# Kernel tuning notes

Hardware: AMD Instinct MI355X
Metric: run time of the kernel (lower is better)

The kernel has to match this reference:

```python
import jax, jax.numpy as jnp
import numpy as np

N, E = 100000, 600000
IN, H = 164, 128
NH = 4  # attention heads over embed_dim H//4 = 32


def layer_norm(x, g, b, eps=1e-5):
    m = x.mean(-1, keepdims=True)
    v = x.var(-1, keepdims=True)
    return (x - m) * jax.lax.rsqrt(v + eps) * g + b


def gcn_conv(x, W, b, src, dst, n):
    # PyG GCNConv: add self-loops, symmetric D^{-1/2}(A+I)D^{-1/2} normalization.
    deg = jnp.ones((n,), x.dtype).at[dst].add(1.0)  # degree of A+I on target nodes
    dinv = jax.lax.rsqrt(deg)
    xw = x @ W  # [n, out]
    msg = xw[src] * (dinv[src] * dinv[dst])[:, None]  # gather + edge-norm
    agg = jax.ops.segment_sum(msg, dst, num_segments=n)  # scatter-add
    agg = agg + xw * (dinv * dinv)[:, None]  # self-loop term
    return agg + b


def mha_seq1(x, Wq, bq, Wk, bk, Wv, bv, Wo, bo):
    # nn.MultiheadAttention with seq_len==1: softmax over a single key -> weights==1.
    dh = x.shape[-1] // NH
    q = (x @ Wq + bq).reshape(-1, NH, dh)
    k = (x @ Wk + bk).reshape(-1, NH, dh)
    v = (x @ Wv + bv).reshape(-1, NH, dh)
    scores = jnp.sum(q * k, -1, keepdims=True) / jnp.sqrt(jnp.float32(dh))  # [n,NH,1]
    attn = jax.nn.softmax(scores[..., None], axis=-1)[..., 0]  # all ones, kept for fidelity
    out = (attn * v).reshape(-1, NH * dh)
    return out @ Wo + bo


def setup_inputs() -> dict:
    key = jax.random.key(0)
    ks = jax.random.split(key, 16)

    def kaiming(k, i, o):
        return jax.random.normal(k, (i, o), jnp.float32) * (2.0 / i) ** 0.5

    Ha, Hb, Hc = H, H // 2, H // 4  # 128, 64, 32
    return {
        "x": jax.random.normal(ks[0], (N, IN), jnp.float32),
        "edge_index": jax.random.randint(ks[1], (2, E), 0, N),
        "Wi": kaiming(ks[2], IN, Ha), "bi": jnp.zeros((Ha,), jnp.float32),
        "g1": jnp.ones((Ha,), jnp.float32), "b1": jnp.zeros((Ha,), jnp.float32),
        "Wg1": kaiming(ks[3], Ha, Ha), "bg1": jnp.zeros((Ha,), jnp.float32),
        "Wg2": kaiming(ks[4], Ha, Hb), "bg2": jnp.zeros((Hb,), jnp.float32),
        "g2": jnp.ones((Hb,), jnp.float32), "b2": jnp.zeros((Hb,), jnp.float32),
        "Wg3": kaiming(ks[5], Hb, Hc), "bg3": jnp.zeros((Hc,), jnp.float32),
        "Wq": kaiming(ks[6], Hc, Hc), "bq": jnp.zeros((Hc,), jnp.float32),
        "Wk": kaiming(ks[7], Hc, Hc), "bk": jnp.zeros((Hc,), jnp.float32),
        "Wv": kaiming(ks[8], Hc, Hc), "bv": jnp.zeros((Hc,), jnp.float32),
        "Wo": kaiming(ks[9], Hc, Hc), "bo": jnp.zeros((Hc,), jnp.float32),
        "Wc1": kaiming(ks[10], Hc, H // 8), "bc1": jnp.zeros((H // 8,), jnp.float32),
        "Wc2": kaiming(ks[11], H // 8, 32), "bc2": jnp.zeros((32,), jnp.float32),
        "Wc3": kaiming(ks[12], 32, 1), "bc3": jnp.zeros((1,), jnp.float32),
    }


def reference(x, edge_index, Wi, bi, g1, b1, Wg1, bg1, Wg2, bg2, g2, b2,
              Wg3, bg3, Wq, bq, Wk, bk, Wv, bv, Wo, bo,
              Wc1, bc1, Wc2, bc2, Wc3, bc3):
    src, dst = edge_index[0], edge_index[1]
    n = x.shape[0]
    # dropout layers are identity in eval mode
    h = layer_norm(jax.nn.relu(x @ Wi + bi), g1, b1)
    h1 = jax.nn.relu(gcn_conv(h, Wg1, bg1, src, dst, n)) + h
    h2 = layer_norm(jax.nn.relu(gcn_conv(h1, Wg2, bg2, src, dst, n)), g2, b2)
    h3 = jax.nn.relu(gcn_conv(h2, Wg3, bg3, src, dst, n))
    h3 = mha_seq1(h3, Wq, bq, Wk, bk, Wv, bv, Wo, bo)
    h3 = jax.nn.relu(h3 @ Wc1 + bc1)
    h3 = jax.nn.relu(h3 @ Wc2 + bc2)
    return (h3 @ Wc3 + bc3)[:, 0]
```

## Files before the change

kernel.cpp:

```cpp
#include <hip/hip_runtime.h>


typedef __attribute__((ext_vector_type(8))) _Float16 f16x8;
typedef __attribute__((ext_vector_type(4))) _Float16 f16x4;
typedef __attribute__((ext_vector_type(4))) float f32x4;

#define GLOAD_LDS16(gp, lp)                                        \
  __builtin_amdgcn_global_load_lds(                                \
      (const __attribute__((address_space(1))) void*)(gp),         \
      (__attribute__((address_space(3))) void*)(lp), 16, 0, 0)

static __device__ __forceinline__ void wait_vm0() {
  asm volatile("s_waitcnt vmcnt(0)" ::: "memory");
}
static __device__ __forceinline__ void wait_vm10() {
  asm volatile("s_waitcnt vmcnt(10)" ::: "memory");
}
static __device__ __forceinline__ void wait_vm5() {
  asm volatile("s_waitcnt vmcnt(5)" ::: "memory");
}
static __device__ __forceinline__ void wait_vm3() {
  asm volatile("s_waitcnt vmcnt(3)" ::: "memory");
}
static __device__ __forceinline__ void wait_lgkm0() {
  asm volatile("s_waitcnt lgkmcnt(0)" ::: "memory");
  __builtin_amdgcn_sched_barrier(0);
}

__global__ void k_count(const int* __restrict__ dst, int* __restrict__ counts, int e) {
  int i = blockIdx.x * blockDim.x + threadIdx.x;
  if (i < e) atomicAdd(&counts[dst[i]], 1);
}

__global__ __launch_bounds__(256) void k_scan_part(
    const int* __restrict__ counts, int* __restrict__ bsums, int n) {
  int tid = threadIdx.x;
  int i0 = blockIdx.x * 1024 + tid * 4;
  int s = 0;
#pragma unroll
  for (int k = 0; k < 4; k++) { int i = i0 + k; if (i < n) s += counts[i]; }
#pragma unroll
  for (int d = 1; d < 64; d <<= 1) s += __shfl_xor(s, d);
  __shared__ int wsum[4];
  int lane = tid & 63, w = tid >> 6;
  if (lane == 0) wsum[w] = s;
  __syncthreads();
  if (tid == 0) bsums[blockIdx.x] = wsum[0] + wsum[1] + wsum[2] + wsum[3];
}

__global__ __launch_bounds__(256) void k_scan_down(
    int* __restrict__ counts, const int* __restrict__ bsums,
    int* __restrict__ offsets, float* __restrict__ dinv, int n, int e, int nb) {
  int tid = threadIdx.x;
  int lane = tid & 63, w = tid >> 6;
  __shared__ int wsum[4], psum[4];
  int pv = (tid < nb && tid < blockIdx.x) ? bsums[tid] : 0;
#pragma unroll
  for (int d = 1; d < 64; d <<= 1) pv += __shfl_xor(pv, d);
  if (lane == 0) psum[w] = pv;
  __syncthreads();
  int blockpref = psum[0] + psum[1] + psum[2] + psum[3];

  int i0 = blockIdx.x * 1024 + tid * 4;
  int c[4]; int tsum = 0;
#pragma unroll
  for (int k = 0; k < 4; k++) { int i = i0 + k; c[k] = (i < n) ? counts[i] : 0; tsum += c[k]; }
  int v = tsum;
#pragma unroll
  for (int d = 1; d < 64; d <<= 1) { int t = __shfl_up(v, d); if (lane >= d) v += t; }
  if (lane == 63) wsum[w] = v;
  __syncthreads();
  int wadd = 0;
#pragma unroll
  for (int q = 0; q < 4; q++) if (q < w) wadd += wsum[q];
  int run = (v - tsum) + wadd + blockpref;
#pragma unroll
  for (int k = 0; k < 4; k++) {
    int i = i0 + k;
    if (i < n) {
      offsets[i] = run;
      dinv[i] = rsqrtf((float)(c[k] + 1));
      counts[i] = 0;
    }
    run += c[k];
  }
  if (blockIdx.x == 0 && tid == 0) offsets[n] = e;
}

__global__ void k_fill(const int* __restrict__ src, const int* __restrict__ dst,
                       const int* __restrict__ offsets, int* __restrict__ cursor,
                       const float* __restrict__ dinv, int2* __restrict__ csr, int e) {
  int i = blockIdx.x * blockDim.x + threadIdx.x;
  if (i >= e) return;
  int s = src[i], d = dst[i];
  int pos = atomicAdd(&cursor[d], 1);
  csr[offsets[d] + pos] = make_int2(s, __float_as_int(dinv[s] * dinv[d]));
}

__device__ __forceinline__ void pack_hi(const float* __restrict__ W,
                                        _Float16* __restrict__ dst,
                                        int K, int N, int u) {
  int lane = u & 63; int rest = u >> 6; int CT = N >> 4;
  int ct = rest % CT, ks = rest / CT;
  int gcol = ct * 16 + (lane & 15);
  int gk0 = ks * 32 + (lane >> 4) * 8;
  size_t o = (size_t)(ks * CT + ct) * 512 + lane * 8;
#pragma unroll
  for (int i = 0; i < 8; i++) {
    float v = (gk0 + i < K) ? W[(size_t)(gk0 + i) * N + gcol] : 0.0f;
    dst[o + i] = (_Float16)v;
  }
}

__global__ void k_setup(const float* __restrict__ Wi, const float* __restrict__ Wg1,
                        const float* __restrict__ Wg2, const float* __restrict__ Wg3,
                        _Float16* __restrict__ pWi, _Float16* __restrict__ pWg1,
                        _Float16* __restrict__ pWg2, _Float16* __restrict__ pWg3,
                        int* __restrict__ counts, float* __restrict__ zp, int n) {
  int b = blockIdx.x;
  if (b < 25) {
    int t = b * 256 + threadIdx.x;
    if (t < 3072) pack_hi(Wi, pWi, 164, 128, t);
    else if (t < 5120) pack_hi(Wg1, pWg1, 128, 128, t - 3072);
    else if (t < 6144) pack_hi(Wg2, pWg2, 128, 64, t - 5120);
    else if (t < 6400) pack_hi(Wg3, pWg3, 64, 32, t - 6144);
  } else {
    if (b == 25 && threadIdx.x < 64) zp[threadIdx.x] = 0.0f;
    int i = (b - 25) * 256 + threadIdx.x;
    if (i < n) counts[i] = 0;
  }
}

__global__ __launch_bounds__(512, 4) void k_gemm_in(
    const float* __restrict__ x, const _Float16* __restrict__ pB,
    const float* __restrict__ bias, const float* __restrict__ gamma,
    const float* __restrict__ beta, const float* __restrict__ zp,
    _Float16* __restrict__ out, int n) {
  constexpr int N = 128, CT = 8, KS = 6;
  __shared__ __align__(16) float sAi[8][2][512];
  int tid = threadIdx.x;
  int lane = tid & 63, w = tid >> 6;
  int rowbase = blockIdx.x * 128 + w * 16;
  const f16x8* Bf = (const f16x8*)pB;

  auto stage = [&](int ks, int buf) {
#pragma unroll
    for (int j = 0; j < 2; j++) {
      int r_ = j * 8 + (lane >> 3);
      int c_ = (lane & 7) ^ (lane >> 3);
      int rg = rowbase + r_;
      bool ok = (rg < n) && (ks < 5 || c_ == 0);
      const void* s = ok ? (const void*)(x + (size_t)rg * 164 + ks * 32 + c_ * 4)
                         : (const void*)zp;
      GLOAD_LDS16(s, &sAi[w][buf][j * 256]);
    }
  };

  f32x4 acc[CT];
#pragma unroll
  for (int c = 0; c < CT; c++) acc[c] = (f32x4)0.0f;

  int rr = lane & 15;
  int c0 = (lane >> 4) * 2;
  int s0 = c0 ^ (rr & 7);
  int s1 = (c0 + 1) ^ (rr & 7);

  f16x8 bfr[2][CT];
#pragma unroll
  for (int c = 0; c < CT; c++) bfr[0][c] = Bf[c * 64 + lane];
  stage(0, 0);

#pragma unroll
  for (int ks = 0; ks < KS; ks++) {
    if (ks + 1 < KS) {
#pragma unroll
      for (int c = 0; c < CT; c++)
        bfr[(ks + 1) & 1][c] = Bf[((ks + 1) * CT + c) * 64 + lane];
      stage(ks + 1, (ks + 1) & 1);
      wait_vm10();
    } else {
      wait_vm0();
    }
    const float* bp = &sAi[w][ks & 1][0];
    float4 u0 = *(const float4*)&bp[rr * 32 + s0 * 4];
    float4 u1 = *(const float4*)&bp[rr * 32 + s1 * 4];
    float v[8] = {u0.x, u0.y, u0.z, u0.w, u1.x, u1.y, u1.z, u1.w};
    f16x8 ah;
#pragma unroll
    for (int i = 0; i < 8; i++) ah[i] = (_Float16)v[i];
#pragma unroll
    for (int c = 0; c < CT; c++)
      acc[c] = __builtin_amdgcn_mfma_f32_16x16x32_f16(ah, bfr[ks & 1][c], acc[c], 0, 0, 0);
  }

  int r0 = (lane >> 4) * 4;
  int li = lane & 15;
  float s1v[4] = {0, 0, 0, 0}, s2v[4] = {0, 0, 0, 0};
#pragma unroll
  for (int c = 0; c < CT; c++) {
    float bb = bias[c * 16 + li];
#pragma unroll
    for (int r = 0; r < 4; r++) {
      float t = acc[c][r] + bb;
      t = t > 0.0f ? t : 0.0f;
      acc[c][r] = t;
      s1v[r] += t;
      s2v[r] += t * t;
    }
  }
#pragma unroll
  for (int m = 1; m < 16; m <<= 1) {
#pragma unroll
    for (int r = 0; r < 4; r++) {
      s1v[r] += __shfl_xor(s1v[r], m);
      s2v[r] += __shfl_xor(s2v[r], m);
    }
  }
  wait_lgkm0();
  _Float16* lr = (_Float16*)&sAi[w][0][0];
#pragma unroll
  for (int c = 0; c < CT; c++) {
    float gv = gamma[c * 16 + li], bv = beta[c * 16 + li];
#pragma unroll
    for (int r = 0; r < 4; r++) {
      float mean = s1v[r] * (1.0f / N);
      float var = s2v[r] * (1.0f / N) - mean * mean;
      float rs = rsqrtf(var + 1e-5f);
      lr[(r0 + r) * 128 + c * 16 + li] =
          (_Float16)((acc[c][r] - mean) * rs * gv + bv);
    }
  }
  wait_lgkm0();
#pragma unroll
  for (int i = 0; i < 4; i++) {
    int chunk = i * 64 + lane;
    int rloc = chunk >> 4;
    int cc = chunk & 15;
    if (rowbase + rloc < n)
      *(f16x8*)&out[(size_t)(rowbase + rloc) * 128 + cc * 8] =
          *(const f16x8*)&lr[chunk * 8];
  }
}

template <int K, int N>
__global__ __launch_bounds__(512, 4) void k_gemm_f16(
    const _Float16* __restrict__ A, const _Float16* __restrict__ pB,
    const float* __restrict__ zp, _Float16* __restrict__ out, int n) {
  constexpr int KS = K / 32, CT = N / 16;
  __shared__ __align__(16) _Float16 sA[8][2][512];
  __shared__ __align__(16) _Float16 sR[8][16 * N];
  int tid = threadIdx.x;
  int lane = tid & 63, w = tid >> 6;
  int rowbase = blockIdx.x * 128 + w * 16;
  const f16x8* Bf = (const f16x8*)pB;

  int r_ = lane >> 2;
  int c_ = (lane & 3) ^ (r_ & 3);
  int rg = rowbase + r_;
  const _Float16* asrc = A + (size_t)rg * K + c_ * 8;
  bool rok = rg < n;

  auto stage = [&](int ks, int buf) {
    const void* s = rok ? (const void*)(asrc + ks * 32) : (const void*)zp;
    GLOAD_LDS16(s, &sA[w][buf][0]);
  };

  f32x4 acc[CT];
#pragma unroll
  for (int c = 0; c < CT; c++) acc[c] = (f32x4)0.0f;

  int rr = lane & 15;
  int slot = (lane >> 4) ^ (rr & 3);

  f16x8 bfr[2][CT];
#pragma unroll
  for (int c = 0; c < CT; c++) bfr[0][c] = Bf[c * 64 + lane];
  stage(0, 0);

#pragma unroll
  for (int ks = 0; ks < KS; ks++) {
    if (ks + 1 < KS) {
#pragma unroll
      for (int c = 0; c < CT; c++)
        bfr[(ks + 1) & 1][c] = Bf[((ks + 1) * CT + c) * 64 + lane];
      stage(ks + 1, (ks + 1) & 1);
      if (CT == 8) wait_vm10(); else if (CT == 4) wait_vm5(); else wait_vm3();
    } else {
      wait_vm0();
    }
    f16x8 av = *(const f16x8*)&sA[w][ks & 1][rr * 32 + slot * 8];
#pragma unroll
    for (int c = 0; c < CT; c++)
      acc[c] = __builtin_amdgcn_mfma_f32_16x16x32_f16(av, bfr[ks & 1][c], acc[c], 0, 0, 0);
  }

  int r0 = (lane >> 4) * 4;
  int li = lane & 15;
  wait_lgkm0();
  _Float16* lr = &sR[w][0];
#pragma unroll
  for (int c = 0; c < CT; c++) {
#pragma unroll
    for (int r = 0; r < 4; r++)
      lr[(r0 + r) * N + c * 16 + li] = (_Float16)acc[c][r];
  }
  wait_lgkm0();
#pragma unroll
  for (int i = 0; i < N / 32; i++) {
    int chunk = i * 64 + lane;
    int rloc = chunk / (N / 8);
    int cc = chunk % (N / 8);
    if (rowbase + rloc < n)
      *(f16x8*)&out[(size_t)(rowbase + rloc) * N + cc * 8] =
          *(const f16x8*)&lr[chunk * 8];
  }
}

template <int OUT_D, int MODE>
__global__ __launch_bounds__(256, 2) void k_gather(
    const int* __restrict__ off, const int2* __restrict__ csr,
    const _Float16* __restrict__ xw, const float* __restrict__ dinv,
    const float* __restrict__ bias, const _Float16* __restrict__ auxh,
    const float* __restrict__ gamma, const float* __restrict__ beta,
    _Float16* __restrict__ out, int n) {
  constexpr int TPN = OUT_D / 4;
  constexpr int NPB = 256 / TPN;
  int tid = threadIdx.x;
  int node = blockIdx.x * NPB + tid / TPN;
  int li = tid % TPN;
  if (node >= n) return;
  int start = off[node], end = off[node + 1];
  float di = dinv[node];
  float d2 = di * di;
  const _Float16* xp = xw + 4 * li;
  f16x4 self = *(const f16x4*)(xp + (size_t)node * OUT_D);
  f16x4 hres;
  if constexpr (MODE == 0)
    hres = *(const f16x4*)(auxh + (size_t)node * OUT_D + 4 * li);
  float a0 = (float)self[0] * d2 + bias[4 * li + 0];
  float a1 = (float)self[1] * d2 + bias[4 * li + 1];
  float a2 = (float)self[2] * d2 + bias[4 * li + 2];
  float a3 = (float)self[3] * d2 + bias[4 * li + 3];
  for (int cb = start; cb < end; cb += TPN) {
    int m = end - cb; if (m > TPN) m = TPN;
    int sv = node; float nv = 0.0f;
    if (li < m) { int2 me = csr[cb + li]; sv = me.x; nv = __int_as_float(me.y); }
    for (int j0 = 0; j0 < m; j0 += 8) {
      int s0 = __shfl(sv, j0 + 0, TPN), s1 = __shfl(sv, j0 + 1, TPN);
      int s2 = __shfl(sv, j0 + 2, TPN), s3 = __shfl(sv, j0 + 3, TPN);
      int s4 = __shfl(sv, j0 + 4, TPN), s5 = __shfl(sv, j0 + 5, TPN);
      int s6 = __shfl(sv, j0 + 6, TPN), s7 = __shfl(sv, j0 + 7, TPN);
      float w0 = __shfl(nv, j0 + 0, TPN), w1 = __shfl(nv, j0 + 1, TPN);
      float w2 = __shfl(nv, j0 + 2, TPN), w3 = __shfl(nv, j0 + 3, TPN);
      float w4 = __shfl(nv, j0 + 4, TPN), w5 = __shfl(nv, j0 + 5, TPN);
      float w6 = __shfl(nv, j0 + 6, TPN), w7 = __shfl(nv, j0 + 7, TPN);
      f16x4 v0 = *(const f16x4*)(xp + (size_t)s0 * OUT_D);
      f16x4 v1 = *(const f16x4*)(xp + (size_t)s1 * OUT_D);
      f16x4 v2 = *(const f16x4*)(xp + (size_t)s2 * OUT_D);
      f16x4 v3 = *(const f16x4*)(xp + (size_t)s3 * OUT_D);
      f16x4 v4 = *(const f16x4*)(xp + (size_t)s4 * OUT_D);
      f16x4 v5 = *(const f16x4*)(xp + (size_t)s5 * OUT_D);
      f16x4 v6 = *(const f16x4*)(xp + (size_t)s6 * OUT_D);
      f16x4 v7 = *(const f16x4*)(xp + (size_t)s7 * OUT_D);
      a0 += (float)v0[0] * w0 + (float)v1[0] * w1 + (float)v2[0] * w2 + (float)v3[0] * w3
          + (float)v4[0] * w4 + (float)v5[0] * w5 + (float)v6[0] * w6 + (float)v7[0] * w7;
      a1 += (float)v0[1] * w0 + (float)v1[1] * w1 + (float)v2[1] * w2 + (float)v3[1] * w3
          + (float)v4[1] * w4 + (float)v5[1] * w5 + (float)v6[1] * w6 + (float)v7[1] * w7;
      a2 += (float)v0[2] * w0 + (float)v1[2] * w1 + (float)v2[2] * w2 + (float)v3[2] * w3
          + (float)v4[2] * w4 + (float)v5[2] * w5 + (float)v6[2] * w6 + (float)v7[2] * w7;
      a3 += (float)v0[3] * w0 + (float)v1[3] * w1 + (float)v2[3] * w2 + (float)v3[3] * w3
          + (float)v4[3] * w4 + (float)v5[3] * w5 + (float)v6[3] * w6 + (float)v7[3] * w7;
    }
  }
  _Float16* po = out + (size_t)node * OUT_D + 4 * li;
  if constexpr (MODE == 0) {
    f16x4 o;
    o[0] = (_Float16)((a0 > 0.0f ? a0 : 0.0f) + (float)hres[0]);
    o[1] = (_Float16)((a1 > 0.0f ? a1 : 0.0f) + (float)hres[1]);
    o[2] = (_Float16)((a2 > 0.0f ? a2 : 0.0f) + (float)hres[2]);
    o[3] = (_Float16)((a3 > 0.0f ? a3 : 0.0f) + (float)hres[3]);
    *(f16x4*)po = o;
  } else if constexpr (MODE == 1) {
    float v0 = a0 > 0.0f ? a0 : 0.0f, v1 = a1 > 0.0f ? a1 : 0.0f;
    float v2 = a2 > 0.0f ? a2 : 0.0f, v3 = a3 > 0.0f ? a3 : 0.0f;
    float s1 = v0 + v1 + v2 + v3;
    float s2 = v0 * v0 + v1 * v1 + v2 * v2 + v3 * v3;
#pragma unroll
    for (int d = 1; d < TPN; d <<= 1) {
      s1 += __shfl_xor(s1, d, TPN);
      s2 += __shfl_xor(s2, d, TPN);
    }
    float m_ = s1 * (1.0f / OUT_D);
    float var = s2 * (1.0f / OUT_D) - m_ * m_;
    float rs = rsqrtf(var + 1e-5f);
    f16x4 o;
    o[0] = (_Float16)((v0 - m_) * rs * gamma[4 * li + 0] + beta[4 * li + 0]);
    o[1] = (_Float16)((v1 - m_) * rs * gamma[4 * li + 1] + beta[4 * li + 1]);
    o[2] = (_Float16)((v2 - m_) * rs * gamma[4 * li + 2] + beta[4 * li + 2]);
    o[3] = (_Float16)((v3 - m_) * rs * gamma[4 * li + 3] + beta[4 * li + 3]);
    *(f16x4*)po = o;
  } else {
    f16x4 o;
    o[0] = (_Float16)a0; o[1] = (_Float16)a1;
    o[2] = (_Float16)a2; o[3] = (_Float16)a3;
    *(f16x4*)po = o;
  }
}

__global__ __launch_bounds__(256) void k_tail(
    const _Float16* __restrict__ agg3, const float* __restrict__ Wv,
    const float* __restrict__ bv, const float* __restrict__ Wo,
    const float* __restrict__ bo, const float* __restrict__ Wc1,
    const float* __restrict__ bc1, const float* __restrict__ Wc2,
    const float* __restrict__ bc2, const float* __restrict__ Wc3,
    const float* __restrict__ bc3, float* __restrict__ out, int n) {
  __shared__ float sWv[1024], sWo[1024], sWc1[512], sWc2[512];
  __shared__ float sbv[32], sbo[32], sbc2[32], sWc3[32], sbc1[16], sbc3[1];
  int tid = threadIdx.x;
  for (int i = tid; i < 1024; i += 256) { sWv[i] = Wv[i]; sWo[i] = Wo[i]; }
  for (int i = tid; i < 512; i += 256) { sWc1[i] = Wc1[i]; sWc2[i] = Wc2[i]; }
  if (tid < 32) { sbv[tid] = bv[tid]; sbo[tid] = bo[tid];
                  sbc2[tid] = bc2[tid]; sWc3[tid] = Wc3[tid]; }
  if (tid < 16) sbc1[tid] = bc1[tid];
  if (tid == 0) sbc3[0] = bc3[0];
  __syncthreads();
  int node = blockIdx.x * blockDim.x + tid;
  if (node >= n) return;
  float a[32];
  const f16x8* row8 = (const f16x8*)(agg3 + (size_t)node * 32);
#pragma unroll
  for (int q = 0; q < 4; q++) {
    f16x8 t = row8[q];
#pragma unroll
    for (int i = 0; i < 8; i++) {
      float f = (float)t[i];
      a[8 * q + i] = f > 0.0f ? f : 0.0f;
    }
  }
  float v[32];
#pragma unroll
  for (int j = 0; j < 32; j++) v[j] = sbv[j];
  for (int k = 0; k < 32; k++) {
#pragma unroll
    for (int j = 0; j < 32; j++) v[j] += a[k] * sWv[k * 32 + j];
  }
  float o[32];
#pragma unroll
  for (int j = 0; j < 32; j++) o[j] = sbo[j];
  for (int k = 0; k < 32; k++) {
#pragma unroll
    for (int j = 0; j < 32; j++) o[j] += v[k] * sWo[k * 32 + j];
  }
  float c1[16];
#pragma unroll
  for (int j = 0; j < 16; j++) c1[j] = sbc1[j];
  for (int k = 0; k < 32; k++) {
#pragma unroll
    for (int j = 0; j < 16; j++) c1[j] += o[k] * sWc1[k * 16 + j];
  }
#pragma unroll
  for (int j = 0; j < 16; j++) c1[j] = c1[j] > 0.0f ? c1[j] : 0.0f;
  float c2[32];
#pragma unroll
  for (int j = 0; j < 32; j++) c2[j] = sbc2[j];
  for (int k = 0; k < 16; k++) {
#pragma unroll
    for (int j = 0; j < 32; j++) c2[j] += c1[k] * sWc2[k * 32 + j];
  }
  float r = sbc3[0];
#pragma unroll
  for (int k = 0; k < 32; k++) {
    float c = c2[k] > 0.0f ? c2[k] : 0.0f;
    r += c * sWc3[k];
  }
  out[node] = r;
}

extern "C" void kernel_launch(void* const* d_in, const int* in_sizes, int n_in,
                              void* d_out, int out_size, void* d_ws, size_t ws_size,
                              hipStream_t stream) {
  const float* x   = (const float*)d_in[0];
  const int* ei    = (const int*)d_in[1];
  const float* Wi  = (const float*)d_in[2];
  const float* bi  = (const float*)d_in[3];
  const float* g1  = (const float*)d_in[4];
  const float* b1  = (const float*)d_in[5];
  const float* Wg1 = (const float*)d_in[6];
  const float* bg1 = (const float*)d_in[7];
  const float* Wg2 = (const float*)d_in[8];
  const float* bg2 = (const float*)d_in[9];
  const float* g2  = (const float*)d_in[10];
  const float* b2  = (const float*)d_in[11];
  const float* Wg3 = (const float*)d_in[12];
  const float* bg3 = (const float*)d_in[13];
  const float* Wv  = (const float*)d_in[18];
  const float* bv  = (const float*)d_in[19];
  const float* Wo  = (const float*)d_in[20];
  const float* bo  = (const float*)d_in[21];
  const float* Wc1 = (const float*)d_in[22];
  const float* bc1 = (const float*)d_in[23];
  const float* Wc2 = (const float*)d_in[24];
  const float* bc2 = (const float*)d_in[25];
  const float* Wc3 = (const float*)d_in[26];
  const float* bc3 = (const float*)d_in[27];

  const int n = in_sizes[0] / 164;
  const int e = in_sizes[1] / 2;
  const int* src = ei;
  const int* dst = ei + e;

  char* ws = (char*)d_ws;
  size_t off = 0;
  auto alloc = [&](size_t bytes) {
    char* p = ws + off;
    off += (bytes + 255) & ~(size_t)255;
    return p;
  };
  _Float16* A     = (_Float16*)alloc((size_t)n * 128 * 2);
  _Float16* B     = (_Float16*)alloc((size_t)n * 128 * 2);
  _Float16* C     = (_Float16*)alloc((size_t)n * 128 * 2);
  float* dinv     = (float*)alloc((size_t)n * 4);
  int*   counts   = (int*)alloc((size_t)n * 4);
  int*   offsets  = (int*)alloc((size_t)(n + 1) * 4);
  int*   bsums    = (int*)alloc(256 * 4);
  int2*  csr      = (int2*)alloc((size_t)e * 8);
  _Float16* pWi   = (_Float16*)alloc(3072 * 16);
  _Float16* pWg1  = (_Float16*)alloc(2048 * 16);
  _Float16* pWg2  = (_Float16*)alloc(1024 * 16);
  _Float16* pWg3  = (_Float16*)alloc(256 * 16);
  float* zp       = (float*)alloc(64 * 4);
  (void)ws_size;

  const int BS = 256;
  const int SB = (n + 1023) / 1024;
  const int GB = (n + 127) / 128;

  k_setup<<<25 + (n + 255) / 256, 256, 0, stream>>>(
      Wi, Wg1, Wg2, Wg3, pWi, pWg1, pWg2, pWg3, counts, zp, n);

  k_count<<<(e + BS - 1) / BS, BS, 0, stream>>>(dst, counts, e);
  k_scan_part<<<SB, 256, 0, stream>>>(counts, bsums, n);
  k_scan_down<<<SB, 256, 0, stream>>>(counts, bsums, offsets, dinv, n, e, SB);
  k_fill<<<(e + BS - 1) / BS, BS, 0, stream>>>(src, dst, offsets, counts, dinv,
                                               csr, e);

  k_gemm_in<<<GB, 512, 0, stream>>>(x, pWi, bi, g1, b1, zp, A, n);

  k_gemm_f16<128, 128><<<GB, 512, 0, stream>>>(A, pWg1, zp, B, n);
  k_gather<128, 0><<<(n + 7) / 8, 256, 0, stream>>>(
      offsets, csr, B, dinv, bg1, A, nullptr, nullptr, C, n);

  k_gemm_f16<128, 64><<<GB, 512, 0, stream>>>(C, pWg2, zp, A, n);
  k_gather<64, 1><<<(n + 15) / 16, 256, 0, stream>>>(
      offsets, csr, A, dinv, bg2, nullptr, g2, b2, B, n);

  k_gemm_f16<64, 32><<<GB, 512, 0, stream>>>(B, pWg3, zp, A, n);
  k_gather<32, 2><<<(n + 31) / 32, 256, 0, stream>>>(
      offsets, csr, A, dinv, bg3, nullptr, nullptr, nullptr, C, n);

  k_tail<<<(n + BS - 1) / BS, BS, 0, stream>>>(
      C, Wv, bv, Wo, bo, Wc1, bc1, Wc2, bc2, Wc3, bc3, (float*)d_out, n);
}
```

Before: 213.8 us.

## Deepen input GEMM prefetch, stage weights in LDS, widen gather vectors

The input GEMM moves to triple-buffered A staging with per-step vmcnt waits, so loads run two K-steps ahead. The f16 GEMMs now stage the whole packed weight matrix and every A K-slice in LDS up front, reuse the A buffer for the output staging, and drop the occupancy hint from 4 to 2. The 128- and 64-wide gathers switch to 8 halves per thread (f16x8 loads), halving threads per node, while the 32-wide gather keeps 4-wide loads. This trades register double-buffering and occupancy for fewer, wider memory transactions and deeper prefetch.

```diff
diff --git a/kernel.cpp b/kernel.cpp
--- a/kernel.cpp
+++ b/kernel.cpp
@@ -4,23 +4,17 @@
 typedef __attribute__((ext_vector_type(8))) _Float16 f16x8;
 typedef __attribute__((ext_vector_type(4))) _Float16 f16x4;
 typedef __attribute__((ext_vector_type(4))) float f32x4;
+
+template <int V> struct IC { static constexpr int value = V; };
 
 #define GLOAD_LDS16(gp, lp)                                        \
   __builtin_amdgcn_global_load_lds(                                \
       (const __attribute__((address_space(1))) void*)(gp),         \
       (__attribute__((address_space(3))) void*)(lp), 16, 0, 0)
 
-static __device__ __forceinline__ void wait_vm0() {
-  asm volatile("s_waitcnt vmcnt(0)" ::: "memory");
-}
-static __device__ __forceinline__ void wait_vm10() {
-  asm volatile("s_waitcnt vmcnt(10)" ::: "memory");
-}
-static __device__ __forceinline__ void wait_vm5() {
-  asm volatile("s_waitcnt vmcnt(5)" ::: "memory");
-}
-static __device__ __forceinline__ void wait_vm3() {
-  asm volatile("s_waitcnt vmcnt(3)" ::: "memory");
+template <int NV>
+static __device__ __forceinline__ void wait_vm() {
+  asm volatile("s_waitcnt vmcnt(%0)" :: "n"(NV) : "memory");
 }
 static __device__ __forceinline__ void wait_lgkm0() {
   asm volatile("s_waitcnt lgkmcnt(0)" ::: "memory");
@@ -136,8 +130,8 @@
     const float* __restrict__ bias, const float* __restrict__ gamma,
     const float* __restrict__ beta, const float* __restrict__ zp,
     _Float16* __restrict__ out, int n) {
-  constexpr int N = 128, CT = 8, KS = 6;
-  __shared__ __align__(16) float sAi[8][2][512];
+  constexpr int N = 128, CT = 8;
+  __shared__ __align__(16) float sAi[8][3][512];
   int tid = threadIdx.x;
   int lane = tid & 63, w = tid >> 6;
   int rowbase = blockIdx.x * 128 + w * 16;
@@ -166,22 +160,22 @@
   int s1 = (c0 + 1) ^ (rr & 7);
 
   f16x8 bfr[2][CT];
+  stage(0, 0);
+  stage(1, 1);
 #pragma unroll
   for (int c = 0; c < CT; c++) bfr[0][c] = Bf[c * 64 + lane];
-  stage(0, 0);
-
-#pragma unroll
-  for (int ks = 0; ks < KS; ks++) {
-    if (ks + 1 < KS) {
+
+  auto step = [&](auto ksc, auto wnc) {
+    constexpr int ks = decltype(ksc)::value;
+    constexpr int WN = decltype(wnc)::value;
+    if constexpr (ks + 1 < 6) {
 #pragma unroll
       for (int c = 0; c < CT; c++)
         bfr[(ks + 1) & 1][c] = Bf[((ks + 1) * CT + c) * 64 + lane];
-      stage(ks + 1, (ks + 1) & 1);
-      wait_vm10();
-    } else {
-      wait_vm0();
-    }
-    const float* bp = &sAi[w][ks & 1][0];
+    }
+    if constexpr (ks + 2 < 6) stage(ks + 2, (ks + 2) % 3);
+    wait_vm<WN>();
+    const float* bp = &sAi[w][ks % 3][0];
     float4 u0 = *(const float4*)&bp[rr * 32 + s0 * 4];
     float4 u1 = *(const float4*)&bp[rr * 32 + s1 * 4];
     float v[8] = {u0.x, u0.y, u0.z, u0.w, u1.x, u1.y, u1.z, u1.w};
@@ -191,7 +185,13 @@
 #pragma unroll
     for (int c = 0; c < CT; c++)
       acc[c] = __builtin_amdgcn_mfma_f32_16x16x32_f16(ah, bfr[ks & 1][c], acc[c], 0, 0, 0);
-  }
+  };
+  step(IC<0>{}, IC<10>{});
+  step(IC<1>{}, IC<12>{});
+  step(IC<2>{}, IC<12>{});
+  step(IC<3>{}, IC<12>{});
+  step(IC<4>{}, IC<10>{});
+  step(IC<5>{}, IC<0>{});
 
   int r0 = (lane >> 4) * 4;
   int li = lane & 15;
@@ -243,61 +243,57 @@
 }
 
 template <int K, int N>
-__global__ __launch_bounds__(512, 4) void k_gemm_f16(
+__global__ __launch_bounds__(512, 2) void k_gemm_f16(
     const _Float16* __restrict__ A, const _Float16* __restrict__ pB,
     const float* __restrict__ zp, _Float16* __restrict__ out, int n) {
   constexpr int KS = K / 32, CT = N / 16;
-  __shared__ __align__(16) _Float16 sA[8][2][512];
-  __shared__ __align__(16) _Float16 sR[8][16 * N];
+  __shared__ __align__(16) _Float16 sB[KS * CT * 512];
+  __shared__ __align__(16) _Float16 sA[8][KS][512];
   int tid = threadIdx.x;
   int lane = tid & 63, w = tid >> 6;
   int rowbase = blockIdx.x * 128 + w * 16;
-  const f16x8* Bf = (const f16x8*)pB;
+
+  for (int u = w; u < KS * CT; u += 8)
+    GLOAD_LDS16(pB + (size_t)u * 512 + lane * 8, &sB[(size_t)u * 512]);
 
   int r_ = lane >> 2;
-  int c_ = (lane & 3) ^ (r_ & 3);
+  int c_ = (lane & 3) ^ ((r_ >> 1) & 3);
   int rg = rowbase + r_;
-  const _Float16* asrc = A + (size_t)rg * K + c_ * 8;
   bool rok = rg < n;
-
-  auto stage = [&](int ks, int buf) {
-    const void* s = rok ? (const void*)(asrc + ks * 32) : (const void*)zp;
-    GLOAD_LDS16(s, &sA[w][buf][0]);
+  for (int ks = 0; ks < KS; ks++) {
+    const void* s = rok ? (const void*)(A + (size_t)rg * K + ks * 32 + c_ * 8)
+                        : (const void*)zp;
+    GLOAD_LDS16(s, &sA[w][ks][0]);
+  }
+  wait_vm<KS>();
+  __builtin_amdgcn_s_barrier();
+
+  f32x4 acc[CT];
+#pragma unroll
+  for (int c = 0; c < CT; c++) acc[c] = (f32x4)0.0f;
+
+  int rr = lane & 15;
+  int slot = (lane >> 4) ^ ((rr >> 1) & 3);
+
+  auto cstep = [&](auto ksc) {
+    constexpr int ks = decltype(ksc)::value;
+    wait_vm<KS - 1 - ks>();
+    f16x8 av = *(const f16x8*)&sA[w][ks][rr * 32 + slot * 8];
+#pragma unroll
+    for (int c = 0; c < CT; c++) {
+      f16x8 b = *(const f16x8*)&sB[(size_t)(ks * CT + c) * 512 + lane * 8];
+      acc[c] = __builtin_amdgcn_mfma_f32_16x16x32_f16(av, b, acc[c], 0, 0, 0);
+    }
   };
-
-  f32x4 acc[CT];
-#pragma unroll
-  for (int c = 0; c < CT; c++) acc[c] = (f32x4)0.0f;
-
-  int rr = lane & 15;
-  int slot = (lane >> 4) ^ (rr & 3);
-
-  f16x8 bfr[2][CT];
-#pragma unroll
-  for (int c = 0; c < CT; c++) bfr[0][c] = Bf[c * 64 + lane];
-  stage(0, 0);
-
-#pragma unroll
-  for (int ks = 0; ks < KS; ks++) {
-    if (ks + 1 < KS) {
-#pragma unroll
-      for (int c = 0; c < CT; c++)
-        bfr[(ks + 1) & 1][c] = Bf[((ks + 1) * CT + c) * 64 + lane];
-      stage(ks + 1, (ks + 1) & 1);
-      if (CT == 8) wait_vm10(); else if (CT == 4) wait_vm5(); else wait_vm3();
-    } else {
-      wait_vm0();
-    }
-    f16x8 av = *(const f16x8*)&sA[w][ks & 1][rr * 32 + slot * 8];
-#pragma unroll
-    for (int c = 0; c < CT; c++)
-      acc[c] = __builtin_amdgcn_mfma_f32_16x16x32_f16(av, bfr[ks & 1][c], acc[c], 0, 0, 0);
-  }
+  cstep(IC<0>{});
+  if constexpr (KS > 1) cstep(IC<1>{});
+  if constexpr (KS > 2) cstep(IC<2>{});
+  if constexpr (KS > 3) cstep(IC<3>{});
 
   int r0 = (lane >> 4) * 4;
   int li = lane & 15;
   wait_lgkm0();
-  _Float16* lr = &sR[w][0];
+  _Float16* lr = &sA[w][0][0];
 #pragma unroll
   for (int c = 0; c < CT; c++) {
 #pragma unroll
@@ -317,14 +313,86 @@
 }
 
 template <int OUT_D, int MODE>
-__global__ __launch_bounds__(256, 2) void k_gather(
+__global__ __launch_bounds__(256, 2) void k_gather8(
     const int* __restrict__ off, const int2* __restrict__ csr,
     const _Float16* __restrict__ xw, const float* __restrict__ dinv,
     const float* __restrict__ bias, const _Float16* __restrict__ auxh,
     const float* __restrict__ gamma, const float* __restrict__ beta,
     _Float16* __restrict__ out, int n) {
-  constexpr int TPN = OUT_D / 4;
+  constexpr int TPN = OUT_D / 8;
   constexpr int NPB = 256 / TPN;
+  int tid = threadIdx.x;
+  int node = blockIdx.x * NPB + tid / TPN;
+  int li = tid % TPN;
+  if (node >= n) return;
+  int start = off[node], end = off[node + 1];
+  float di = dinv[node];
+  float d2 = di * di;
+  const _Float16* xp = xw + 8 * li;
+  f16x8 self = *(const f16x8*)(xp + (size_t)node * OUT_D);
+  f16x8 hres;
+  if constexpr (MODE == 0)
+    hres = *(const f16x8*)(auxh + (size_t)node * OUT_D + 8 * li);
+  float a[8];
+#pragma unroll
+  for (int q = 0; q < 8; q++) a[q] = (float)self[q] * d2 + bias[8 * li + q];
+  for (int cb = start; cb < end; cb += TPN) {
+    int m = end - cb; if (m > TPN) m = TPN;
+    int sv = node; float nv = 0.0f;
+    if (li < m) { int2 me = csr[cb + li]; sv = me.x; nv = __int_as_float(me.y); }
+    for (int j0 = 0; j0 < m; j0 += 8) {
+      int s[8]; float wv[8];
+#pragma unroll
+      for (int q = 0; q < 8; q++) {
+        s[q] = __shfl(sv, j0 + q, TPN);
+        wv[q] = __shfl(nv, j0 + q, TPN);
+      }
+      f16x8 v[8];
+#pragma unroll
+      for (int q = 0; q < 8; q++) v[q] = *(const f16x8*)(xp + (size_t)s[q] * OUT_D);
+#pragma unroll
+      for (int q = 0; q < 8; q++) {
+#pragma unroll
+        for (int c = 0; c < 8; c++) a[c] += (float)v[q][c] * wv[q];
+      }
+    }
+  }
+  _Float16* po = out + (size_t)node * OUT_D + 8 * li;
+  if constexpr (MODE == 0) {
+    f16x8 o;
+#pragma unroll
+    for (int q = 0; q < 8; q++)
+      o[q] = (_Float16)((a[q] > 0.0f ? a[q] : 0.0f) + (float)hres[q]);
+    *(f16x8*)po = o;
+  } else {
+    float s1 = 0.0f, s2 = 0.0f;
+#pragma unroll
+    for (int q = 0; q < 8; q++) {
+      a[q] = a[q] > 0.0f ? a[q] : 0.0f;
+      s1 += a[q];
+      s2 += a[q] * a[q];
+    }
+#pragma unroll
+    for (int d = 1; d < TPN; d <<= 1) {
+      s1 += __shfl_xor(s1, d, TPN);
+      s2 += __shfl_xor(s2, d, TPN);
+    }
+    float m_ = s1 * (1.0f / OUT_D);
+    float var = s2 * (1.0f / OUT_D) - m_ * m_;
+    float rs = rsqrtf(var + 1e-5f);
+    f16x8 o;
+#pragma unroll
+    for (int q = 0; q < 8; q++)
+      o[q] = (_Float16)((a[q] - m_) * rs * gamma[8 * li + q] + beta[8 * li + q]);
+    *(f16x8*)po = o;
+  }
+}
+
+__global__ __launch_bounds__(256, 2) void k_gather3(
+    const int* __restrict__ off, const int2* __restrict__ csr,
+    const _Float16* __restrict__ xw, const float* __restrict__ dinv,
+    const float* __restrict__ bias, _Float16* __restrict__ out, int n) {
+  constexpr int OUT_D = 32, TPN = 8, NPB = 32;
   int tid = threadIdx.x;
   int node = blockIdx.x * NPB + tid / TPN;
   int li = tid % TPN;
@@ -334,9 +402,6 @@
   float d2 = di * di;
   const _Float16* xp = xw + 4 * li;
   f16x4 self = *(const f16x4*)(xp + (size_t)node * OUT_D);
-  f16x4 hres;
-  if constexpr (MODE == 0)
-    hres = *(const f16x4*)(auxh + (size_t)node * OUT_D + 4 * li);
   float a0 = (float)self[0] * d2 + bias[4 * li + 0];
   float a1 = (float)self[1] * d2 + bias[4 * li + 1];
   float a2 = (float)self[2] * d2 + bias[4 * li + 2];
@@ -346,65 +411,28 @@
     int sv = node; float nv = 0.0f;
     if (li < m) { int2 me = csr[cb + li]; sv = me.x; nv = __int_as_float(me.y); }
     for (int j0 = 0; j0 < m; j0 += 8) {
-      int s0 = __shfl(sv, j0 + 0, TPN), s1 = __shfl(sv, j0 + 1, TPN);
-      int s2 = __shfl(sv, j0 + 2, TPN), s3 = __shfl(sv, j0 + 3, TPN);
-      int s4 = __shfl(sv, j0 + 4, TPN), s5 = __shfl(sv, j0 + 5, TPN);
-      int s6 = __shfl(sv, j0 + 6, TPN), s7 = __shfl(sv, j0 + 7, TPN);
-      float w0 = __shfl(nv, j0 + 0, TPN), w1 = __shfl(nv, j0 + 1, TPN);
-      float w2 = __shfl(nv, j0 + 2, TPN), w3 = __shfl(nv, j0 + 3, TPN);
-      float w4 = __shfl(nv, j0 + 4, TPN), w5 = __shfl(nv, j0 + 5, TPN);
-      float w6 = __shfl(nv, j0 + 6, TPN), w7 = __shfl(nv, j0 + 7, TPN);
-      f16x4 v0 = *(const f16x4*)(xp + (size_t)s0 * OUT_D);
-      f16x4 v1 = *(const f16x4*)(xp + (size_t)s1 * OUT_D);
-      f16x4 v2 = *(const f16x4*)(xp + (size_t)s2 * OUT_D);
-      f16x4 v3 = *(const f16x4*)(xp + (size_t)s3 * OUT_D);
-      f16x4 v4 = *(const f16x4*)(xp + (size_t)s4 * OUT_D);
-      f16x4 v5 = *(const f16x4*)(xp + (size_t)s5 * OUT_D);
-      f16x4 v6 = *(const f16x4*)(xp + (size_t)s6 * OUT_D);
-      f16x4 v7 = *(const f16x4*)(xp + (size_t)s7 * OUT_D);
-      a0 += (float)v0[0] * w0 + (float)v1[0] * w1 + (float)v2[0] * w2 + (float)v3[0] * w3
-          + (float)v4[0] * w4 + (float)v5[0] * w5 + (float)v6[0] * w6 + (float)v7[0] * w7;
-      a1 += (float)v0[1] * w0 + (float)v1[1] * w1 + (float)v2[1] * w2 + (float)v3[1] * w3
-          + (float)v4[1] * w4 + (float)v5[1] * w5 + (float)v6[1] * w6 + (float)v7[1] * w7;
-      a2 += (float)v0[2] * w0 + (float)v1[2] * w1 + (float)v2[2] * w2 + (float)v3[2] * w3
-          + (float)v4[2] * w4 + (float)v5[2] * w5 + (float)v6[2] * w6 + (float)v7[2] * w7;
-      a3 += (float)v0[3] * w0 + (float)v1[3] * w1 + (float)v2[3] * w2 + (float)v3[3] * w3
-          + (float)v4[3] * w4 + (float)v5[3] * w5 + (float)v6[3] * w6 + (float)v7[3] * w7;
-    }
-  }
-  _Float16* po = out + (size_t)node * OUT_D + 4 * li;
-  if constexpr (MODE == 0) {
-    f16x4 o;
-    o[0] = (_Float16)((a0 > 0.0f ? a0 : 0.0f) + (float)hres[0]);
-    o[1] = (_Float16)((a1 > 0.0f ? a1 : 0.0f) + (float)hres[1]);
-    o[2] = (_Float16)((a2 > 0.0f ? a2 : 0.0f) + (float)hres[2]);
-    o[3] = (_Float16)((a3 > 0.0f ? a3 : 0.0f) + (float)hres[3]);
-    *(f16x4*)po = o;
-  } else if constexpr (MODE == 1) {
-    float v0 = a0 > 0.0f ? a0 : 0.0f, v1 = a1 > 0.0f ? a1 : 0.0f;
-    float v2 = a2 > 0.0f ? a2 : 0.0f, v3 = a3 > 0.0f ? a3 : 0.0f;
-    float s1 = v0 + v1 + v2 + v3;
-    float s2 = v0 * v0 + v1 * v1 + v2 * v2 + v3 * v3;
-#pragma unroll
-    for (int d = 1; d < TPN; d <<= 1) {
-      s1 += __shfl_xor(s1, d, TPN);
-      s2 += __shfl_xor(s2, d, TPN);
-    }
-    float m_ = s1 * (1.0f / OUT_D);
-    float var = s2 * (1.0f / OUT_D) - m_ * m_;
-    float rs = rsqrtf(var + 1e-5f);
-    f16x4 o;
-    o[0] = (_Float16)((v0 - m_) * rs * gamma[4 * li + 0] + beta[4 * li + 0]);
-    o[1] = (_Float16)((v1 - m_) * rs * gamma[4 * li + 1] + beta[4 * li + 1]);
-    o[2] = (_Float16)((v2 - m_) * rs * gamma[4 * li + 2] + beta[4 * li + 2]);
-    o[3] = (_Float16)((v3 - m_) * rs * gamma[4 * li + 3] + beta[4 * li + 3]);
-    *(f16x4*)po = o;
-  } else {
-    f16x4 o;
-    o[0] = (_Float16)a0; o[1] = (_Float16)a1;
-    o[2] = (_Float16)a2; o[3] = (_Float16)a3;
-    *(f16x4*)po = o;
-  }
+      int s[8]; float wv[8];
+#pragma unroll
+      for (int q = 0; q < 8; q++) {
+        s[q] = __shfl(sv, j0 + q, TPN);
+        wv[q] = __shfl(nv, j0 + q, TPN);
+      }
+      f16x4 v[8];
+#pragma unroll
+      for (int q = 0; q < 8; q++) v[q] = *(const f16x4*)(xp + (size_t)s[q] * OUT_D);
+#pragma unroll
+      for (int q = 0; q < 8; q++) {
+        a0 += (float)v[q][0] * wv[q];
+        a1 += (float)v[q][1] * wv[q];
+        a2 += (float)v[q][2] * wv[q];
+        a3 += (float)v[q][3] * wv[q];
+      }
+    }
+  }
+  f16x4 o;
+  o[0] = (_Float16)a0; o[1] = (_Float16)a1;
+  o[2] = (_Float16)a2; o[3] = (_Float16)a3;
+  *(f16x4*)(out + (size_t)node * OUT_D + 4 * li) = o;
 }
 
 __global__ __launch_bounds__(256) void k_tail(
@@ -547,16 +575,16 @@
   k_gemm_in<<<GB, 512, 0, stream>>>(x, pWi, bi, g1, b1, zp, A, n);
 
   k_gemm_f16<128, 128><<<GB, 512, 0, stream>>>(A, pWg1, zp, B, n);
-  k_gather<128, 0><<<(n + 7) / 8, 256, 0, stream>>>(
+  k_gather8<128, 0><<<(n + 15) / 16, 256, 0, stream>>>(
       offsets, csr, B, dinv, bg1, A, nullptr, nullptr, C, n);
 
   k_gemm_f16<128, 64><<<GB, 512, 0, stream>>>(C, pWg2, zp, A, n);
-  k_gather<64, 1><<<(n + 15) / 16, 256, 0, stream>>>(
+  k_gather8<64, 1><<<(n + 31) / 32, 256, 0, stream>>>(
       offsets, csr, A, dinv, bg2, nullptr, g2, b2, B, n);
 
   k_gemm_f16<64, 32><<<GB, 512, 0, stream>>>(B, pWg3, zp, A, n);
-  k_gather<32, 2><<<(n + 31) / 32, 256, 0, stream>>>(
-      offsets, csr, A, dinv, bg3, nullptr, nullptr, nullptr, C, n);
+  k_gather3<<<(n + 31) / 32, 256, 0, stream>>>(
+      offsets, csr, A, dinv, bg3, C, n);
 
   k_tail<<<(n + BS - 1) / BS, BS, 0, stream>>>(
       C, Wv, bv, Wo, bo, Wc1, bc1, Wc2, bc2, Wc3, bc3, (float*)d_out, n);
```

Result: no change. 214.2 us (+0.2%).
